# Kernel optimization log

Hardware: AMD Instinct MI355X
Metric: run time of the kernel (lower is better)

## Reference

```python
import jax, jax.numpy as jnp
import numpy as np

C_IN, C_KEY, C_VAL, HEADS = 64, 64, 64, 4


def _bilinear_one(img, py, px):
    # img: [C,H,W]; py,px: [H,W] float sampling coords. Zero padding outside.
    H, W = img.shape[1], img.shape[2]
    y0 = jnp.floor(py); x0 = jnp.floor(px)
    wy1 = py - y0; wy0 = 1.0 - wy1
    wx1 = px - x0; wx0 = 1.0 - wx1

    def gather(yi, xi):
        yc = jnp.clip(yi, 0, H - 1).astype(jnp.int32)
        xc = jnp.clip(xi, 0, W - 1).astype(jnp.int32)
        m = ((yi >= 0) & (yi <= H - 1) & (xi >= 0) & (xi <= W - 1)).astype(img.dtype)
        return img[:, yc, xc] * m  # [C,H,W]

    return (gather(y0, x0) * (wy0 * wx0) + gather(y0, x0 + 1) * (wy0 * wx1)
            + gather(y0 + 1, x0) * (wy1 * wx0) + gather(y0 + 1, x0 + 1) * (wy1 * wx1))


def deform_conv1x1(x, off_w, off_b, w):
    # x: [N,C,H,W]; off_w: [2,C]; off_b: [2]; w: [O,C]
    N, C, H, W = x.shape
    off = jnp.einsum('nchw,oc->nohw', x, off_w) + off_b[None, :, None, None]
    py = jnp.arange(H, dtype=x.dtype)[:, None] + off[:, 0]  # [N,H,W]
    px = jnp.arange(W, dtype=x.dtype)[None, :] + off[:, 1]
    sampled = jax.vmap(_bilinear_one)(x, py, px)  # [N,C,H,W]
    return jnp.einsum('nchw,oc->nohw', sampled, w)


def setup_inputs() -> dict:
    key = jax.random.key(0)
    ks = jax.random.split(key, 12)
    N, H, W = 4, 256, 256
    sc = 1.0 / np.sqrt(C_IN)
    inp = {
        'x': jax.random.normal(ks[0], (N, C_IN, H, W), jnp.float32),
        'k_off_w': jax.random.normal(ks[1], (2, C_IN), jnp.float32) * 0.05,
        'k_off_b': jnp.zeros((2,), jnp.float32),
        'k_w': jax.random.normal(ks[2], (C_KEY, C_IN), jnp.float32) * sc,
        'q_off_w': jax.random.normal(ks[3], (2, C_IN), jnp.float32) * 0.05,
        'q_off_b': jnp.zeros((2,), jnp.float32),
        'q_w': jax.random.normal(ks[4], (C_KEY, C_IN), jnp.float32) * sc,
        'v_off_w': jax.random.normal(ks[5], (2, C_IN), jnp.float32) * 0.05,
        'v_off_b': jnp.zeros((2,), jnp.float32),
        'v_w': jax.random.normal(ks[6], (C_VAL, C_IN), jnp.float32) * sc,
        'rp_w': jax.random.normal(ks[7], (C_IN, C_VAL), jnp.float32) / np.sqrt(C_VAL),
        'rp_b': jax.random.normal(ks[8], (C_IN,), jnp.float32) * 0.01,
    }
    return inp


def reference(x, k_off_w, k_off_b, k_w, q_off_w, q_off_b, q_w,
              v_off_w, v_off_b, v_w, rp_w, rp_b):
    N, _, H, W = x.shape
    S = H * W
    dk, dv = C_KEY // HEADS, C_VAL // HEADS
    keys = deform_conv1x1(x, k_off_w, k_off_b, k_w).reshape(N, HEADS, dk, S)
    queries = deform_conv1x1(x, q_off_w, q_off_b, q_w).reshape(N, HEADS, dk, S)
    values = deform_conv1x1(x, v_off_w, v_off_b, v_w).reshape(N, HEADS, dv, S)
    key_sm = jax.nn.softmax(keys, axis=-1)        # softmax over spatial (dim=2)
    query_sm = jax.nn.softmax(queries, axis=2)    # softmax over channel (dim=1)
    # context = key @ value^T : [dk,dv] per (n,head)
    context = jnp.einsum('nhks,nhvs->nhkv', key_sm, values)
    # attended = context^T @ query : [dv,S]
    attended = jnp.einsum('nhkv,nhks->nhvs', context, query_sm)
    aggregated = attended.reshape(N, C_VAL, H, W)
    return jnp.einsum('nvhw,ov->nohw', aggregated, rp_w) + rp_b[None, :, None, None]
```

## Files before the change

kernel.cpp:

```cpp
#include <hip/hip_runtime.h>
#include <math.h>

#define CI 64
#define HH 256
#define WW 256
#define SS (HH*WW)

typedef __attribute__((ext_vector_type(8))) short bf16x8;
typedef __attribute__((ext_vector_type(4))) float f32x4;

__global__ void k_zero(float* __restrict__ ws) {
  int i = blockIdx.x * 256 + threadIdx.x;
  if (i < 4352) ws[i] = 0.f;
}

__device__ __forceinline__ ushort f2bf(float f) {
  unsigned u = __float_as_uint(f);
  u += 0x7FFF + ((u >> 16) & 1);
  return (ushort)(u >> 16);
}
__device__ __forceinline__ float bf2f(ushort h) { return __uint_as_float(((unsigned)h) << 16); }
__device__ __forceinline__ void split(float x, ushort& h, ushort& l) {
  h = f2bf(x); l = f2bf(x - bf2f(h));
}

__device__ __forceinline__ bf16x8 ld8(const ushort* t, int row, int c8) {
  return *reinterpret_cast<const bf16x8*>(t + row * 64 + ((c8 ^ (row & 7)) << 3));
}
__device__ __forceinline__ int swi(int row, int col) {
  return row * 64 + ((((col >> 3) ^ (row & 7)) << 3) | (col & 7));
}

union B8 { bf16x8 v; ushort u[8]; };

struct WFrag { bf16x8 h[2]; bf16x8 l[2]; };
__device__ __forceinline__ WFrag load_w(const float* __restrict__ W, int h16, int lane) {
  WFrag f;
  int m = lane & 15, q = lane >> 4;
#pragma unroll
  for (int ks = 0; ks < 2; ks++) {
    const float* p = W + (size_t)(h16 + m) * 64 + ks * 32 + q * 8;
    float4 f0 = *(const float4*)p, f1 = *(const float4*)(p + 4);
    float vals[8] = {f0.x, f0.y, f0.z, f0.w, f1.x, f1.y, f1.z, f1.w};
    B8 hh, ll;
#pragma unroll
    for (int j = 0; j < 8; j++) { ushort a, b; split(vals[j], a, b); hh.u[j] = a; ll.u[j] = b; }
    f.h[ks] = hh.v; f.l[ks] = ll.v;
  }
  return f;
}

__device__ __forceinline__ void gemm_wave(const WFrag& w, const ushort* Th, const ushort* Tl,
                                          int lane, f32x4 acc[4]) {
  int m = lane & 15, q = lane >> 4;
#pragma unroll
  for (int nt = 0; nt < 4; nt++) {
#pragma unroll
    for (int ks = 0; ks < 2; ks++) {
      bf16x8 bh = ld8(Th, nt * 16 + m, ks * 4 + q);
      bf16x8 bl = ld8(Tl, nt * 16 + m, ks * 4 + q);
      acc[nt] = __builtin_amdgcn_mfma_f32_16x16x32_bf16(w.h[ks], bh, acc[nt], 0, 0, 0);
      acc[nt] = __builtin_amdgcn_mfma_f32_16x16x32_bf16(w.h[ks], bl, acc[nt], 0, 0, 0);
      acc[nt] = __builtin_amdgcn_mfma_f32_16x16x32_bf16(w.l[ks], bh, acc[nt], 0, 0, 0);
    }
  }
}

__device__ __forceinline__ void bilin_params(float py, float px, float w[4], int a[4]) {
  float y0f = floorf(py), x0f = floorf(px);
  float wy1 = py - y0f, wy0 = 1.f - wy1;
  float wx1 = px - x0f, wx0 = 1.f - wx1;
  int iy0 = (int)y0f, ix0 = (int)x0f;
  int iy1 = iy0 + 1, ix1 = ix0 + 1;
  float vy0 = (iy0 >= 0 && iy0 < HH) ? 1.f : 0.f;
  float vy1 = (iy1 >= 0 && iy1 < HH) ? 1.f : 0.f;
  float vx0 = (ix0 >= 0 && ix0 < WW) ? 1.f : 0.f;
  float vx1 = (ix1 >= 0 && ix1 < WW) ? 1.f : 0.f;
  int cy0 = min(max(iy0, 0), HH - 1), cy1 = min(max(iy1, 0), HH - 1);
  int cx0 = min(max(ix0, 0), WW - 1), cx1 = min(max(ix1, 0), WW - 1);
  w[0] = wy0 * wx0 * vy0 * vx0;
  w[1] = wy0 * wx1 * vy0 * vx1;
  w[2] = wy1 * wx0 * vy1 * vx0;
  w[3] = wy1 * wx1 * vy1 * vx1;
  a[0] = cy0 * WW + cx0;  a[1] = cy0 * WW + cx1;
  a[2] = cy1 * WW + cx0;  a[3] = cy1 * WW + cx1;
}

__device__ __forceinline__ void sample16(const float* __restrict__ Xb,
                                         const float* __restrict__ pw,
                                         const int* __restrict__ pa,
                                         ushort* __restrict__ Sh, ushort* __restrict__ Sl,
                                         int pix, int cg) {
  float w0 = pw[0 * 64 + pix], w1 = pw[1 * 64 + pix], w2 = pw[2 * 64 + pix], w3 = pw[3 * 64 + pix];
  int a0 = pa[0 * 64 + pix], a1 = pa[1 * 64 + pix], a2 = pa[2 * 64 + pix], a3 = pa[3 * 64 + pix];
#pragma unroll 2
  for (int half = 0; half < 2; half++) {
    B8 hh, ll;
#pragma unroll
    for (int j = 0; j < 8; j++) {
      const float* Xc = Xb + (size_t)(half * 8 + j) * SS;
      float v = w0 * Xc[a0] + w1 * Xc[a1] + w2 * Xc[a2] + w3 * Xc[a3];
      ushort a, b; split(v, a, b); hh.u[j] = a; ll.u[j] = b;
    }
    int idx = pix * 64 + ((((cg * 2 + half) ^ (pix & 7))) << 3);
    *reinterpret_cast<bf16x8*>(Sh + idx) = hh.v;
    *reinterpret_cast<bf16x8*>(Sl + idx) = ll.v;
  }
}

__global__ __launch_bounds__(256, 4) void k_context(
    const float* __restrict__ x,
    const float* __restrict__ kow, const float* __restrict__ kob,
    const float* __restrict__ kw,
    const float* __restrict__ vow, const float* __restrict__ vob,
    const float* __restrict__ vw,
    float* __restrict__ num, float* __restrict__ den) {
  __shared__ ushort Sh[4096], Sl[4096];
  __shared__ ushort Vh[4096], Vl[4096];
  float* red = (float*)Vh;
  float* pws = (float*)Vl;
  int*   pas = (int*)Vl + 512;

  const int t = threadIdx.x;
  const int bp = ((blockIdx.x & 7) << 9) | (blockIdx.x >> 3);
  const int xt = bp & 3, yrow = (bp >> 2) & 255, n = bp >> 10;
  const int xb = xt * 64;
  const int s0 = yrow * WW + xb;
  const float* xn = x + (size_t)n * CI * SS;
  const int pix = t & 63;
  const int cg = t >> 6;
  const int cgu = __builtin_amdgcn_readfirstlane(cg);
  const int m = pix & 15, q = pix >> 4;
  const float* Xb = xn + (size_t)(cgu * 16) * SS;

  {
    const float* xc = Xb + s0 + pix;
    float p0 = 0, p1 = 0, p2 = 0, p3 = 0;
#pragma unroll 8
    for (int i = 0; i < 16; i++) {
      float xv = xc[(size_t)i * SS];
      p0 += kow[cgu * 16 + i] * xv;
      p1 += kow[64 + cgu * 16 + i] * xv;
      p2 += vow[cgu * 16 + i] * xv;
      p3 += vow[64 + cgu * 16 + i] * xv;
    }
    red[(0 * 4 + cg) * 64 + pix] = p0;
    red[(1 * 4 + cg) * 64 + pix] = p1;
    red[(2 * 4 + cg) * 64 + pix] = p2;
    red[(3 * 4 + cg) * 64 + pix] = p3;
  }
  __syncthreads();
  if (t < 128) {
    int p = t & 63, sel = t >> 6, qb = sel * 2;
    float oy = red[((qb + 0) * 4 + 0) * 64 + p] + red[((qb + 0) * 4 + 1) * 64 + p] +
               red[((qb + 0) * 4 + 2) * 64 + p] + red[((qb + 0) * 4 + 3) * 64 + p];
    float ox = red[((qb + 1) * 4 + 0) * 64 + p] + red[((qb + 1) * 4 + 1) * 64 + p] +
               red[((qb + 1) * 4 + 2) * 64 + p] + red[((qb + 1) * 4 + 3) * 64 + p];
    const float* ob = sel ? vob : kob;
    float py = (float)yrow + oy + ob[0];
    float px = (float)(xb + p) + ox + ob[1];
    float w4[4]; int a4[4];
    bilin_params(py, px, w4, a4);
#pragma unroll
    for (int qq = 0; qq < 4; qq++) { pws[(sel * 4 + qq) * 64 + p] = w4[qq]; pas[(sel * 4 + qq) * 64 + p] = a4[qq]; }
  }
  __syncthreads();
  sample16(Xb, pws, pas, Sh, Sl, pix, cg);
  WFrag wk = load_w(kw, cgu * 16, pix);
  __syncthreads();
  float ek[16];
  {
    f32x4 acc[4] = {{0,0,0,0},{0,0,0,0},{0,0,0,0},{0,0,0,0}};
    gemm_wave(wk, Sh, Sl, pix, acc);
#pragma unroll
    for (int nt = 0; nt < 4; nt++)
#pragma unroll
      for (int r = 0; r < 4; r++) ek[nt * 4 + r] = __expf(acc[nt][r]);
    float s[4];
#pragma unroll
    for (int r = 0; r < 4; r++) s[r] = ek[r] + ek[4 + r] + ek[8 + r] + ek[12 + r];
#pragma unroll
    for (int mask = 1; mask < 16; mask <<= 1)
#pragma unroll
      for (int r = 0; r < 4; r++) s[r] += __shfl_xor(s[r], mask);
    if (m == 0) {
#pragma unroll
      for (int r = 0; r < 4; r++) atomicAdd(&den[n * 64 + cgu * 16 + q * 4 + r], s[r]);
    }
  }
  __syncthreads();
  sample16(Xb, pws + 4 * 64, pas + 4 * 64, Sh, Sl, pix, cg);
  WFrag wv = load_w(vw, cgu * 16, pix);
  __syncthreads();
  f32x4 vacc[4] = {{0,0,0,0},{0,0,0,0},{0,0,0,0},{0,0,0,0}};
  gemm_wave(wv, Sh, Sl, pix, vacc);
  __syncthreads();
#pragma unroll
  for (int nt = 0; nt < 4; nt++) {
    int px = nt * 16 + m;
#pragma unroll
    for (int r = 0; r < 4; r++) {
      int row = cgu * 16 + q * 4 + r;
      int ix = swi(row, px);
      ushort a, b;
      split(ek[nt * 4 + r], a, b);  Sh[ix] = a; Sl[ix] = b;
      split(vacc[nt][r], a, b);     Vh[ix] = a; Vl[ix] = b;
    }
  }
  __syncthreads();
  {
    f32x4 c = {0, 0, 0, 0};
#pragma unroll
    for (int ks = 0; ks < 2; ks++) {
      bf16x8 ah = ld8(Sh, cgu * 16 + m, ks * 4 + q);
      bf16x8 al = ld8(Sl, cgu * 16 + m, ks * 4 + q);
      bf16x8 bh = ld8(Vh, cgu * 16 + m, ks * 4 + q);
      bf16x8 bl = ld8(Vl, cgu * 16 + m, ks * 4 + q);
      c = __builtin_amdgcn_mfma_f32_16x16x32_bf16(ah, bh, c, 0, 0, 0);
      c = __builtin_amdgcn_mfma_f32_16x16x32_bf16(ah, bl, c, 0, 0, 0);
      c = __builtin_amdgcn_mfma_f32_16x16x32_bf16(al, bh, c, 0, 0, 0);
    }
    float* nb = num + n * 1024 + cgu * 256;
#pragma unroll
    for (int r = 0; r < 4; r++) atomicAdd(&nb[(q * 4 + r) * 16 + m], c[r]);
  }
}

__global__ __launch_bounds__(256, 4) void k_output(
    const float* __restrict__ x,
    const float* __restrict__ qow, const float* __restrict__ qob,
    const float* __restrict__ qw,
    const float* __restrict__ rw, const float* __restrict__ rb,
    const float* __restrict__ num, const float* __restrict__ den,
    float* __restrict__ out) {
  __shared__ ushort Sh[4096], Sl[4096];
  __shared__ float ctxs[1024];
  __shared__ float pws2[256];
  __shared__ int   pas2[256];
  float* red2 = (float*)Sh;

  const int t = threadIdx.x;
  const int bp = ((blockIdx.x & 7) << 9) | (blockIdx.x >> 3);
  const int xt = bp & 3, yrow = (bp >> 2) & 255, n = bp >> 10;
  const int xb = xt * 64;
  const int s0 = yrow * WW + xb;
  const float* xn = x + (size_t)n * CI * SS;
  const int pix = t & 63;
  const int cg = t >> 6;
  const int cgu = __builtin_amdgcn_readfirstlane(cg);
  const int m = pix & 15, q = pix >> 4;
  const float* Xb = xn + (size_t)(cgu * 16) * SS;

#pragma unroll
  for (int i = 0; i < 4; i++) {
    int e = t + i * 256;
    ctxs[e] = num[n * 1024 + e] / den[n * 64 + (e >> 4)];
  }

  {
    const float* xc = Xb + s0 + pix;
    float p0 = 0, p1 = 0;
#pragma unroll 8
    for (int i = 0; i < 16; i++) {
      float xv = xc[(size_t)i * SS];
      p0 += qow[cgu * 16 + i] * xv;
      p1 += qow[64 + cgu * 16 + i] * xv;
    }
    red2[cg * 64 + pix] = p0;
    red2[(4 + cg) * 64 + pix] = p1;
  }
  __syncthreads();
  if (t < 64) {
    float oy = red2[0 * 64 + t] + red2[1 * 64 + t] + red2[2 * 64 + t] + red2[3 * 64 + t];
    float ox = red2[4 * 64 + t] + red2[5 * 64 + t] + red2[6 * 64 + t] + red2[7 * 64 + t];
    float py = (float)yrow + oy + qob[0];
    float px = (float)(xb + t) + ox + qob[1];
    float w4[4]; int a4[4];
    bilin_params(py, px, w4, a4);
#pragma unroll
    for (int qq = 0; qq < 4; qq++) { pws2[qq * 64 + t] = w4[qq]; pas2[qq * 64 + t] = a4[qq]; }
  }
  __syncthreads();
  sample16(Xb, pws2, pas2, Sh, Sl, pix, cg);
  WFrag wq = load_w(qw, cgu * 16, pix);
  __syncthreads();
  float qsm[16];
  {
    f32x4 acc[4] = {{0,0,0,0},{0,0,0,0},{0,0,0,0},{0,0,0,0}};
    gemm_wave(wq, Sh, Sl, pix, acc);
#pragma unroll
    for (int nt = 0; nt < 4; nt++) {
      float mx = fmaxf(fmaxf(acc[nt][0], acc[nt][1]), fmaxf(acc[nt][2], acc[nt][3]));
      mx = fmaxf(mx, __shfl_xor(mx, 16));
      mx = fmaxf(mx, __shfl_xor(mx, 32));
      float e[4]; float ssum = 0.f;
#pragma unroll
      for (int r = 0; r < 4; r++) { e[r] = __expf(acc[nt][r] - mx); ssum += e[r]; }
      ssum += __shfl_xor(ssum, 16);
      ssum += __shfl_xor(ssum, 32);
      float inv = 1.f / ssum;
#pragma unroll
      for (int r = 0; r < 4; r++) qsm[nt * 4 + r] = e[r] * inv;
    }
  }
  __syncthreads();
#pragma unroll
  for (int nt = 0; nt < 4; nt++) {
    int px = nt * 16 + m;
#pragma unroll
    for (int r = 0; r < 4; r++) {
      int ix = swi(px, cgu * 16 + q * 4 + r);
      ushort a, b; split(qsm[nt * 4 + r], a, b);
      Sh[ix] = a; Sl[ix] = b;
    }
  }
  __syncthreads();
  f32x4 att[4];
  {
    bf16x8 ah, al;
    B8 hh, ll;
#pragma unroll
    for (int j = 0; j < 8; j++) {
      float cv = (q < 2) ? ctxs[cgu * 256 + (q * 8 + j) * 16 + m] : 0.f;
      ushort a, b; split(cv, a, b); hh.u[j] = a; ll.u[j] = b;
    }
    ah = hh.v; al = ll.v;
    bf16x8 z = {0, 0, 0, 0, 0, 0, 0, 0};
#pragma unroll
    for (int nt = 0; nt < 4; nt++) {
      bf16x8 bh = (q < 2) ? ld8(Sh, nt * 16 + m, cgu * 2 + q) : z;
      bf16x8 bl = (q < 2) ? ld8(Sl, nt * 16 + m, cgu * 2 + q) : z;
      f32x4 c = {0, 0, 0, 0};
      c = __builtin_amdgcn_mfma_f32_16x16x32_bf16(ah, bh, c, 0, 0, 0);
      c = __builtin_amdgcn_mfma_f32_16x16x32_bf16(ah, bl, c, 0, 0, 0);
      c = __builtin_amdgcn_mfma_f32_16x16x32_bf16(al, bh, c, 0, 0, 0);
      att[nt] = c;
    }
  }
  __syncthreads();
#pragma unroll
  for (int nt = 0; nt < 4; nt++) {
    int px = nt * 16 + m;
#pragma unroll
    for (int r = 0; r < 4; r++) {
      int ix = swi(px, cgu * 16 + q * 4 + r);
      ushort a, b; split(att[nt][r], a, b);
      Sh[ix] = a; Sl[ix] = b;
    }
  }
  WFrag wr = load_w(rw, cgu * 16, pix);
  float rbv[4];
#pragma unroll
  for (int r = 0; r < 4; r++) rbv[r] = rb[cgu * 16 + q * 4 + r];
  __syncthreads();
  {
    f32x4 oacc[4] = {{0,0,0,0},{0,0,0,0},{0,0,0,0},{0,0,0,0}};
    gemm_wave(wr, Sh, Sl, pix, oacc);
#pragma unroll
    for (int nt = 0; nt < 4; nt++) {
#pragma unroll
      for (int r = 0; r < 4; r++) {
        int o = cgu * 16 + q * 4 + r;
        out[(size_t)(n * 64 + o) * SS + s0 + nt * 16 + m] = oacc[nt][r] + rbv[r];
      }
    }
  }
}

extern "C" void kernel_launch(void* const* d_in, const int* in_sizes, int n_in,
                              void* d_out, int out_size, void* d_ws, size_t ws_size,
                              hipStream_t stream) {
  const float* x   = (const float*)d_in[0];
  const float* kow = (const float*)d_in[1];
  const float* kob = (const float*)d_in[2];
  const float* kw  = (const float*)d_in[3];
  const float* qow = (const float*)d_in[4];
  const float* qob = (const float*)d_in[5];
  const float* qw  = (const float*)d_in[6];
  const float* vow = (const float*)d_in[7];
  const float* vob = (const float*)d_in[8];
  const float* vw  = (const float*)d_in[9];
  const float* rw  = (const float*)d_in[10];
  const float* rb  = (const float*)d_in[11];
  float* out = (float*)d_out;
  float* wsf = (float*)d_ws;
  float* num = wsf;
  float* den = wsf + 4096;

  hipLaunchKernelGGL(k_zero, dim3(17), dim3(256), 0, stream, wsf);
  hipLaunchKernelGGL(k_context, dim3(4096), dim3(256), 0, stream,
                     x, kow, kob, kw, vow, vob, vw, num, den);
  hipLaunchKernelGGL(k_output, dim3(4096), dim3(256), 0, stream,
                     x, qow, qob, qw, rw, rb, num, den, out);
}
```

Before: 295.8 us.

## Process a full image row per block, looping over x-tiles with hoisted weights

Each block now covers a whole 256-pixel row by looping over four 64-pixel tiles instead of handling one tile, with grids reduced to 1024 blocks. Weight fragments, bias and the context matrix are loaded once per block and reused across tiles. Context and denominator partials accumulate in registers so there is one set of atomics per block rather than per tile. The key and value samples now go into separate LDS buffers and their two GEMMs run back to back, with fewer barriers. The cost is more LDS per block and fewer blocks to hide latency, which may lower occupancy.

```diff
diff --git a/kernel.cpp b/kernel.cpp
--- a/kernel.cpp
+++ b/kernel.cpp
@@ -117,15 +117,13 @@
     float* __restrict__ num, float* __restrict__ den) {
   __shared__ ushort Sh[4096], Sl[4096];
   __shared__ ushort Vh[4096], Vl[4096];
-  float* red = (float*)Vh;
-  float* pws = (float*)Vl;
-  int*   pas = (int*)Vl + 512;
+  __shared__ float red[1024];
+  __shared__ float pws[512];
+  __shared__ int   pas[512];
 
   const int t = threadIdx.x;
-  const int bp = ((blockIdx.x & 7) << 9) | (blockIdx.x >> 3);
-  const int xt = bp & 3, yrow = (bp >> 2) & 255, n = bp >> 10;
-  const int xb = xt * 64;
-  const int s0 = yrow * WW + xb;
+  const int bp = ((blockIdx.x & 7) << 7) | (blockIdx.x >> 3);
+  const int yrow = bp & 255, n = bp >> 8;
   const float* xn = x + (size_t)n * CI * SS;
   const int pix = t & 63;
   const int cg = t >> 6;
@@ -133,96 +131,100 @@
   const int m = pix & 15, q = pix >> 4;
   const float* Xb = xn + (size_t)(cgu * 16) * SS;
 
-  {
-    const float* xc = Xb + s0 + pix;
-    float p0 = 0, p1 = 0, p2 = 0, p3 = 0;
+  const WFrag wk = load_w(kw, cgu * 16, pix);
+  const WFrag wv = load_w(vw, cgu * 16, pix);
+  f32x4 cacc = {0, 0, 0, 0};
+  float dacc[4] = {0, 0, 0, 0};
+
+  for (int xt = 0; xt < 4; ++xt) {
+    const int xb = xt * 64;
+    const int s0 = yrow * WW + xb;
+
+    {
+      const float* xc = Xb + s0 + pix;
+      float p0 = 0, p1 = 0, p2 = 0, p3 = 0;
 #pragma unroll 8
-    for (int i = 0; i < 16; i++) {
-      float xv = xc[(size_t)i * SS];
-      p0 += kow[cgu * 16 + i] * xv;
-      p1 += kow[64 + cgu * 16 + i] * xv;
-      p2 += vow[cgu * 16 + i] * xv;
-      p3 += vow[64 + cgu * 16 + i] * xv;
-    }
-    red[(0 * 4 + cg) * 64 + pix] = p0;
-    red[(1 * 4 + cg) * 64 + pix] = p1;
-    red[(2 * 4 + cg) * 64 + pix] = p2;
-    red[(3 * 4 + cg) * 64 + pix] = p3;
-  }
-  __syncthreads();
-  if (t < 128) {
-    int p = t & 63, sel = t >> 6, qb = sel * 2;
-    float oy = red[((qb + 0) * 4 + 0) * 64 + p] + red[((qb + 0) * 4 + 1) * 64 + p] +
-               red[((qb + 0) * 4 + 2) * 64 + p] + red[((qb + 0) * 4 + 3) * 64 + p];
-    float ox = red[((qb + 1) * 4 + 0) * 64 + p] + red[((qb + 1) * 4 + 1) * 64 + p] +
-               red[((qb + 1) * 4 + 2) * 64 + p] + red[((qb + 1) * 4 + 3) * 64 + p];
-    const float* ob = sel ? vob : kob;
-    float py = (float)yrow + oy + ob[0];
-    float px = (float)(xb + p) + ox + ob[1];
-    float w4[4]; int a4[4];
-    bilin_params(py, px, w4, a4);
-#pragma unroll
-    for (int qq = 0; qq < 4; qq++) { pws[(sel * 4 + qq) * 64 + p] = w4[qq]; pas[(sel * 4 + qq) * 64 + p] = a4[qq]; }
-  }
-  __syncthreads();
-  sample16(Xb, pws, pas, Sh, Sl, pix, cg);
-  WFrag wk = load_w(kw, cgu * 16, pix);
-  __syncthreads();
-  float ek[16];
-  {
-    f32x4 acc[4] = {{0,0,0,0},{0,0,0,0},{0,0,0,0},{0,0,0,0}};
-    gemm_wave(wk, Sh, Sl, pix, acc);
-#pragma unroll
-    for (int nt = 0; nt < 4; nt++)
-#pragma unroll
-      for (int r = 0; r < 4; r++) ek[nt * 4 + r] = __expf(acc[nt][r]);
-    float s[4];
-#pragma unroll
-    for (int r = 0; r < 4; r++) s[r] = ek[r] + ek[4 + r] + ek[8 + r] + ek[12 + r];
-#pragma unroll
-    for (int mask = 1; mask < 16; mask <<= 1)
-#pragma unroll
-      for (int r = 0; r < 4; r++) s[r] += __shfl_xor(s[r], mask);
-    if (m == 0) {
-#pragma unroll
-      for (int r = 0; r < 4; r++) atomicAdd(&den[n * 64 + cgu * 16 + q * 4 + r], s[r]);
-    }
-  }
-  __syncthreads();
-  sample16(Xb, pws + 4 * 64, pas + 4 * 64, Sh, Sl, pix, cg);
-  WFrag wv = load_w(vw, cgu * 16, pix);
-  __syncthreads();
-  f32x4 vacc[4] = {{0,0,0,0},{0,0,0,0},{0,0,0,0},{0,0,0,0}};
-  gemm_wave(wv, Sh, Sl, pix, vacc);
-  __syncthreads();
-#pragma unroll
-  for (int nt = 0; nt < 4; nt++) {
-    int px = nt * 16 + m;
-#pragma unroll
-    for (int r = 0; r < 4; r++) {
-      int row = cgu * 16 + q * 4 + r;
-      int ix = swi(row, px);
-      ushort a, b;
-      split(ek[nt * 4 + r], a, b);  Sh[ix] = a; Sl[ix] = b;
-      split(vacc[nt][r], a, b);     Vh[ix] = a; Vl[ix] = b;
-    }
-  }
-  __syncthreads();
-  {
-    f32x4 c = {0, 0, 0, 0};
+      for (int i = 0; i < 16; i++) {
+        float xv = xc[(size_t)i * SS];
+        p0 += kow[cgu * 16 + i] * xv;
+        p1 += kow[64 + cgu * 16 + i] * xv;
+        p2 += vow[cgu * 16 + i] * xv;
+        p3 += vow[64 + cgu * 16 + i] * xv;
+      }
+      red[(0 * 4 + cg) * 64 + pix] = p0;
+      red[(1 * 4 + cg) * 64 + pix] = p1;
+      red[(2 * 4 + cg) * 64 + pix] = p2;
+      red[(3 * 4 + cg) * 64 + pix] = p3;
+    }
+    __syncthreads();
+    if (t < 128) {
+      int p = t & 63, sel = t >> 6, qb = sel * 2;
+      float oy = red[((qb + 0) * 4 + 0) * 64 + p] + red[((qb + 0) * 4 + 1) * 64 + p] +
+                 red[((qb + 0) * 4 + 2) * 64 + p] + red[((qb + 0) * 4 + 3) * 64 + p];
+      float ox = red[((qb + 1) * 4 + 0) * 64 + p] + red[((qb + 1) * 4 + 1) * 64 + p] +
+                 red[((qb + 1) * 4 + 2) * 64 + p] + red[((qb + 1) * 4 + 3) * 64 + p];
+      const float* ob = sel ? vob : kob;
+      float py = (float)yrow + oy + ob[0];
+      float px = (float)(xb + p) + ox + ob[1];
+      float w4[4]; int a4[4];
+      bilin_params(py, px, w4, a4);
+#pragma unroll
+      for (int qq = 0; qq < 4; qq++) { pws[(sel * 4 + qq) * 64 + p] = w4[qq]; pas[(sel * 4 + qq) * 64 + p] = a4[qq]; }
+    }
+    __syncthreads();
+    sample16(Xb, pws, pas, Sh, Sl, pix, cg);
+    sample16(Xb, pws + 256, pas + 256, Vh, Vl, pix, cg);
+    __syncthreads();
+    float ek[16];
+    f32x4 vacc[4] = {{0,0,0,0},{0,0,0,0},{0,0,0,0},{0,0,0,0}};
+    {
+      f32x4 acc[4] = {{0,0,0,0},{0,0,0,0},{0,0,0,0},{0,0,0,0}};
+      gemm_wave(wk, Sh, Sl, pix, acc);
+      gemm_wave(wv, Vh, Vl, pix, vacc);
+#pragma unroll
+      for (int nt = 0; nt < 4; nt++)
+#pragma unroll
+        for (int r = 0; r < 4; r++) ek[nt * 4 + r] = __expf(acc[nt][r]);
+#pragma unroll
+      for (int r = 0; r < 4; r++) dacc[r] += ek[r] + ek[4 + r] + ek[8 + r] + ek[12 + r];
+    }
+    __syncthreads();
+#pragma unroll
+    for (int nt = 0; nt < 4; nt++) {
+      int px = nt * 16 + m;
+#pragma unroll
+      for (int r = 0; r < 4; r++) {
+        int row = cgu * 16 + q * 4 + r;
+        int ix = swi(row, px);
+        ushort a, b;
+        split(ek[nt * 4 + r], a, b);  Sh[ix] = a; Sl[ix] = b;
+        split(vacc[nt][r], a, b);     Vh[ix] = a; Vl[ix] = b;
+      }
+    }
+    __syncthreads();
 #pragma unroll
     for (int ks = 0; ks < 2; ks++) {
       bf16x8 ah = ld8(Sh, cgu * 16 + m, ks * 4 + q);
       bf16x8 al = ld8(Sl, cgu * 16 + m, ks * 4 + q);
       bf16x8 bh = ld8(Vh, cgu * 16 + m, ks * 4 + q);
       bf16x8 bl = ld8(Vl, cgu * 16 + m, ks * 4 + q);
-      c = __builtin_amdgcn_mfma_f32_16x16x32_bf16(ah, bh, c, 0, 0, 0);
-      c = __builtin_amdgcn_mfma_f32_16x16x32_bf16(ah, bl, c, 0, 0, 0);
-      c = __builtin_amdgcn_mfma_f32_16x16x32_bf16(al, bh, c, 0, 0, 0);
-    }
+      cacc = __builtin_amdgcn_mfma_f32_16x16x32_bf16(ah, bh, cacc, 0, 0, 0);
+      cacc = __builtin_amdgcn_mfma_f32_16x16x32_bf16(ah, bl, cacc, 0, 0, 0);
+      cacc = __builtin_amdgcn_mfma_f32_16x16x32_bf16(al, bh, cacc, 0, 0, 0);
+    }
+  }
+  {
     float* nb = num + n * 1024 + cgu * 256;
 #pragma unroll
-    for (int r = 0; r < 4; r++) atomicAdd(&nb[(q * 4 + r) * 16 + m], c[r]);
+    for (int r = 0; r < 4; r++) atomicAdd(&nb[(q * 4 + r) * 16 + m], cacc[r]);
+#pragma unroll
+    for (int mask = 1; mask < 16; mask <<= 1)
+#pragma unroll
+      for (int r = 0; r < 4; r++) dacc[r] += __shfl_xor(dacc[r], mask);
+    if (m == 0) {
+#pragma unroll
+      for (int r = 0; r < 4; r++) atomicAdd(&den[n * 64 + cgu * 16 + q * 4 + r], dacc[r]);
+    }
   }
 }
 
@@ -234,16 +236,15 @@
     const float* __restrict__ num, const float* __restrict__ den,
     float* __restrict__ out) {
   __shared__ ushort Sh[4096], Sl[4096];
+  __shared__ ushort Qh[4096], Ql[4096];
   __shared__ float ctxs[1024];
   __shared__ float pws2[256];
   __shared__ int   pas2[256];
-  float* red2 = (float*)Sh;
+  float* red2 = (float*)Qh;
 
   const int t = threadIdx.x;
-  const int bp = ((blockIdx.x & 7) << 9) | (blockIdx.x >> 3);
-  const int xt = bp & 3, yrow = (bp >> 2) & 255, n = bp >> 10;
-  const int xb = xt * 64;
-  const int s0 = yrow * WW + xb;
+  const int bp = ((blockIdx.x & 7) << 7) | (blockIdx.x >> 3);
+  const int yrow = bp & 255, n = bp >> 8;
   const float* xn = x + (size_t)n * CI * SS;
   const int pix = t & 63;
   const int cg = t >> 6;
@@ -251,117 +252,113 @@
   const int m = pix & 15, q = pix >> 4;
   const float* Xb = xn + (size_t)(cgu * 16) * SS;
 
+  const WFrag wq = load_w(qw, cgu * 16, pix);
+  const WFrag wr = load_w(rw, cgu * 16, pix);
+  float rbv[4];
+#pragma unroll
+  for (int r = 0; r < 4; r++) rbv[r] = rb[cgu * 16 + q * 4 + r];
+
 #pragma unroll
   for (int i = 0; i < 4; i++) {
     int e = t + i * 256;
     ctxs[e] = num[n * 1024 + e] / den[n * 64 + (e >> 4)];
   }
-
+  __syncthreads();
+  bf16x8 cah, cal;
   {
-    const float* xc = Xb + s0 + pix;
-    float p0 = 0, p1 = 0;
-#pragma unroll 8
-    for (int i = 0; i < 16; i++) {
-      float xv = xc[(size_t)i * SS];
-      p0 += qow[cgu * 16 + i] * xv;
-      p1 += qow[64 + cgu * 16 + i] * xv;
-    }
-    red2[cg * 64 + pix] = p0;
-    red2[(4 + cg) * 64 + pix] = p1;
-  }
-  __syncthreads();
-  if (t < 64) {
-    float oy = red2[0 * 64 + t] + red2[1 * 64 + t] + red2[2 * 64 + t] + red2[3 * 64 + t];
-    float ox = red2[4 * 64 + t] + red2[5 * 64 + t] + red2[6 * 64 + t] + red2[7 * 64 + t];
-    float py = (float)yrow + oy + qob[0];
-    float px = (float)(xb + t) + ox + qob[1];
-    float w4[4]; int a4[4];
-    bilin_params(py, px, w4, a4);
-#pragma unroll
-    for (int qq = 0; qq < 4; qq++) { pws2[qq * 64 + t] = w4[qq]; pas2[qq * 64 + t] = a4[qq]; }
-  }
-  __syncthreads();
-  sample16(Xb, pws2, pas2, Sh, Sl, pix, cg);
-  WFrag wq = load_w(qw, cgu * 16, pix);
-  __syncthreads();
-  float qsm[16];
-  {
-    f32x4 acc[4] = {{0,0,0,0},{0,0,0,0},{0,0,0,0},{0,0,0,0}};
-    gemm_wave(wq, Sh, Sl, pix, acc);
-#pragma unroll
-    for (int nt = 0; nt < 4; nt++) {
-      float mx = fmaxf(fmaxf(acc[nt][0], acc[nt][1]), fmaxf(acc[nt][2], acc[nt][3]));
-      mx = fmaxf(mx, __shfl_xor(mx, 16));
-      mx = fmaxf(mx, __shfl_xor(mx, 32));
-      float e[4]; float ssum = 0.f;
-#pragma unroll
-      for (int r = 0; r < 4; r++) { e[r] = __expf(acc[nt][r] - mx); ssum += e[r]; }
-      ssum += __shfl_xor(ssum, 16);
-      ssum += __shfl_xor(ssum, 32);
-      float inv = 1.f / ssum;
-#pragma unroll
-      for (int r = 0; r < 4; r++) qsm[nt * 4 + r] = e[r] * inv;
-    }
-  }
-  __syncthreads();
-#pragma unroll
-  for (int nt = 0; nt < 4; nt++) {
-    int px = nt * 16 + m;
-#pragma unroll
-    for (int r = 0; r < 4; r++) {
-      int ix = swi(px, cgu * 16 + q * 4 + r);
-      ushort a, b; split(qsm[nt * 4 + r], a, b);
-      Sh[ix] = a; Sl[ix] = b;
-    }
-  }
-  __syncthreads();
-  f32x4 att[4];
-  {
-    bf16x8 ah, al;
     B8 hh, ll;
 #pragma unroll
     for (int j = 0; j < 8; j++) {
       float cv = (q < 2) ? ctxs[cgu * 256 + (q * 8 + j) * 16 + m] : 0.f;
       ushort a, b; split(cv, a, b); hh.u[j] = a; ll.u[j] = b;
     }
-    ah = hh.v; al = ll.v;
-    bf16x8 z = {0, 0, 0, 0, 0, 0, 0, 0};
-#pragma unroll
-    for (int nt = 0; nt < 4; nt++) {
-      bf16x8 bh = (q < 2) ? ld8(Sh, nt * 16 + m, cgu * 2 + q) : z;
-      bf16x8 bl = (q < 2) ? ld8(Sl, nt * 16 + m, cgu * 2 + q) : z;
-      f32x4 c = {0, 0, 0, 0};
-      c = __builtin_amdgcn_mfma_f32_16x16x32_bf16(ah, bh, c, 0, 0, 0);
-      c = __builtin_amdgcn_mfma_f32_16x16x32_bf16(ah, bl, c, 0, 0, 0);
-      c = __builtin_amdgcn_mfma_f32_16x16x32_bf16(al, bh, c, 0, 0, 0);
-      att[nt] = c;
-    }
-  }
-  __syncthreads();
-#pragma unroll
-  for (int nt = 0; nt < 4; nt++) {
-    int px = nt * 16 + m;
-#pragma unroll
-    for (int r = 0; r < 4; r++) {
-      int ix = swi(px, cgu * 16 + q * 4 + r);
-      ushort a, b; split(att[nt][r], a, b);
-      Sh[ix] = a; Sl[ix] = b;
-    }
-  }
-  WFrag wr = load_w(rw, cgu * 16, pix);
-  float rbv[4];
-#pragma unroll
-  for (int r = 0; r < 4; r++) rbv[r] = rb[cgu * 16 + q * 4 + r];
-  __syncthreads();
-  {
-    f32x4 oacc[4] = {{0,0,0,0},{0,0,0,0},{0,0,0,0},{0,0,0,0}};
-    gemm_wave(wr, Sh, Sl, pix, oacc);
-#pragma unroll
-    for (int nt = 0; nt < 4; nt++) {
-#pragma unroll
-      for (int r = 0; r < 4; r++) {
-        int o = cgu * 16 + q * 4 + r;
-        out[(size_t)(n * 64 + o) * SS + s0 + nt * 16 + m] = oacc[nt][r] + rbv[r];
+    cah = hh.v; cal = ll.v;
+  }
+
+  for (int xt = 0; xt < 4; ++xt) {
+    const int xb = xt * 64;
+    const int s0 = yrow * WW + xb;
+
+    {
+      const float* xc = Xb + s0 + pix;
+      float p0 = 0, p1 = 0;
+#pragma unroll 8
+      for (int i = 0; i < 16; i++) {
+        float xv = xc[(size_t)i * SS];
+        p0 += qow[cgu * 16 + i] * xv;
+        p1 += qow[64 + cgu * 16 + i] * xv;
+      }
+      red2[cg * 64 + pix] = p0;
+      red2[(4 + cg) * 64 + pix] = p1;
+    }
+    __syncthreads();
+    if (t < 64) {
+      float oy = red2[0 * 64 + t] + red2[1 * 64 + t] + red2[2 * 64 + t] + red2[3 * 64 + t];
+      float ox = red2[4 * 64 + t] + red2[5 * 64 + t] + red2[6 * 64 + t] + red2[7 * 64 + t];
+      float py = (float)yrow + oy + qob[0];
+      float px = (float)(xb + t) + ox + qob[1];
+      float w4[4]; int a4[4];
+      bilin_params(py, px, w4, a4);
+#pragma unroll
+      for (int qq = 0; qq < 4; qq++) { pws2[qq * 64 + t] = w4[qq]; pas2[qq * 64 + t] = a4[qq]; }
+    }
+    __syncthreads();
+    sample16(Xb, pws2, pas2, Sh, Sl, pix, cg);
+    __syncthreads();
+    {
+      f32x4 acc[4] = {{0,0,0,0},{0,0,0,0},{0,0,0,0},{0,0,0,0}};
+      gemm_wave(wq, Sh, Sl, pix, acc);
+#pragma unroll
+      for (int nt = 0; nt < 4; nt++) {
+        float mx = fmaxf(fmaxf(acc[nt][0], acc[nt][1]), fmaxf(acc[nt][2], acc[nt][3]));
+        mx = fmaxf(mx, __shfl_xor(mx, 16));
+        mx = fmaxf(mx, __shfl_xor(mx, 32));
+        float e[4]; float ssum = 0.f;
+#pragma unroll
+        for (int r = 0; r < 4; r++) { e[r] = __expf(acc[nt][r] - mx); ssum += e[r]; }
+        ssum += __shfl_xor(ssum, 16);
+        ssum += __shfl_xor(ssum, 32);
+        float inv = 1.f / ssum;
+        int px = nt * 16 + m;
+#pragma unroll
+        for (int r = 0; r < 4; r++) {
+          int ix = swi(px, cgu * 16 + q * 4 + r);
+          ushort a, b; split(e[r] * inv, a, b);
+          Qh[ix] = a; Ql[ix] = b;
+        }
+      }
+    }
+    __syncthreads();
+    {
+      bf16x8 z = {0, 0, 0, 0, 0, 0, 0, 0};
+#pragma unroll
+      for (int nt = 0; nt < 4; nt++) {
+        bf16x8 bh = (q < 2) ? ld8(Qh, nt * 16 + m, cgu * 2 + q) : z;
+        bf16x8 bl = (q < 2) ? ld8(Ql, nt * 16 + m, cgu * 2 + q) : z;
+        f32x4 c = {0, 0, 0, 0};
+        c = __builtin_amdgcn_mfma_f32_16x16x32_bf16(cah, bh, c, 0, 0, 0);
+        c = __builtin_amdgcn_mfma_f32_16x16x32_bf16(cah, bl, c, 0, 0, 0);
+        c = __builtin_amdgcn_mfma_f32_16x16x32_bf16(cal, bh, c, 0, 0, 0);
+        int px = nt * 16 + m;
+#pragma unroll
+        for (int r = 0; r < 4; r++) {
+          int ix = swi(px, cgu * 16 + q * 4 + r);
+          ushort a, b; split(c[r], a, b);
+          Sh[ix] = a; Sl[ix] = b;
+        }
+      }
+    }
+    __syncthreads();
+    {
+      f32x4 oacc[4] = {{0,0,0,0},{0,0,0,0},{0,0,0,0},{0,0,0,0}};
+      gemm_wave(wr, Sh, Sl, pix, oacc);
+#pragma unroll
+      for (int nt = 0; nt < 4; nt++) {
+#pragma unroll
+        for (int r = 0; r < 4; r++) {
+          int o = cgu * 16 + q * 4 + r;
+          out[(size_t)(n * 64 + o) * SS + s0 + nt * 16 + m] = oacc[nt][r] + rbv[r];
+        }
       }
     }
   }
@@ -388,8 +385,8 @@
   float* den = wsf + 4096;
 
   hipLaunchKernelGGL(k_zero, dim3(17), dim3(256), 0, stream, wsf);
-  hipLaunchKernelGGL(k_context, dim3(4096), dim3(256), 0, stream,
+  hipLaunchKernelGGL(k_context, dim3(1024), dim3(256), 0, stream,
                      x, kow, kob, kw, vow, vob, vw, num, den);
-  hipLaunchKernelGGL(k_output, dim3(4096), dim3(256), 0, stream,
+  hipLaunchKernelGGL(k_output, dim3(1024), dim3(256), 0, stream,
                      x, qow, qob, qw, rw, rb, num, den, out);
 }
```

Result: slower. 309.1 us (+4.5%).
